# Kernel optimization log

Measured on AMD Instinct MI355X. Metric: run time of the kernel, lower is better.

## Reference

```python
import jax, jax.numpy as jnp
import numpy as np

IN_SIZE = 65536
HIDDEN = 128
D_STEPS = 64   # nd_actions[0]
N_ACT = 512    # nd_actions[1]


def setup_inputs() -> dict:
    key = jax.random.key(0)
    ks = jax.random.split(key, 7)
    s = 1.0 / np.sqrt(HIDDEN)  # torch LSTMCell/Linear init scale (uniform); use scaled normal
    return {
        "x": jax.random.normal(ks[0], (IN_SIZE,), jnp.float32),
        "w_ih": jax.random.normal(ks[1], (4 * HIDDEN, IN_SIZE), jnp.float32) * s,
        "w_hh": jax.random.normal(ks[2], (4 * HIDDEN, HIDDEN), jnp.float32) * s,
        "b_ih": jax.random.normal(ks[3], (4 * HIDDEN,), jnp.float32) * s,
        "b_hh": jax.random.normal(ks[4], (4 * HIDDEN,), jnp.float32) * s,
        "w_lin": jax.random.normal(ks[5], (N_ACT, HIDDEN), jnp.float32) * s,
        "b_lin": jax.random.normal(ks[6], (N_ACT,), jnp.float32) * s,
    }


def reference(x, w_ih, w_hh, b_ih, b_hh, w_lin, b_lin):
    # x is constant across the D steps, so its gate contribution is computed once.
    ihx = w_ih @ x + b_ih + b_hh  # (4H,)
    h0 = jnp.zeros((HIDDEN,), x.dtype)
    c0 = jnp.zeros((HIDDEN,), x.dtype)

    def step(carry, _):
        h, c = carry
        gates = ihx + w_hh @ h  # (4H,)
        i, f, g, o = jnp.split(gates, 4)  # torch LSTMCell gate order: i, f, g, o
        c = jax.nn.sigmoid(f) * c + jax.nn.sigmoid(i) * jnp.tanh(g)
        h = jax.nn.sigmoid(o) * jnp.tanh(c)
        logits = w_lin @ h + b_lin  # (N,)
        return (h, c), logits

    _, action_probs = jax.lax.scan(step, (h0, c0), None, length=D_STEPS)
    return action_probs  # (D, N)
```

## Files before the change

kernel.cpp:

```cpp
#include <hip/hip_runtime.h>
#include <hip/hip_bf16.h>

#define IN_SIZE 65536
#define HIDDEN 128
#define D_STEPS 64
#define N_ACT 512

typedef _Float16 half2_ __attribute__((ext_vector_type(2)));
typedef _Float16 half8_ __attribute__((ext_vector_type(8)));

__device__ __forceinline__ float dot2f(half2_ a, half2_ b, float c) {
#if __has_builtin(__builtin_amdgcn_fdot2)
    return __builtin_amdgcn_fdot2(a, b, c, false);
#else
    return c + (float)a[0] * (float)b[0] + (float)a[1] * (float)b[1];
#endif
}

__global__ __launch_bounds__(256) void k_ihx(const float* __restrict__ w_ih,
                                             const float* __restrict__ x,
                                             float* __restrict__ partials) {
    int bid = blockIdx.x;
    int rp = bid >> 3;
    int ck = bid & 7;
    int t = threadIdx.x;
    int r0 = 2 * rp, r1 = 2 * rp + 1;
    const float4* xp = (const float4*)(x + ck * 8192);
    const float4* w0 = (const float4*)(w_ih + (size_t)r0 * IN_SIZE + ck * 8192);
    const float4* w1 = (const float4*)(w_ih + (size_t)r1 * IN_SIZE + ck * 8192);

    float4 xv[8];
#pragma unroll
    for (int i = 0; i < 8; ++i) xv[i] = xp[t + i * 256];

    float a0 = 0.f, a1 = 0.f;
#pragma unroll
    for (int i = 0; i < 8; ++i) {
        float4 w4 = w0[t + i * 256];
        a0 += w4.x * xv[i].x + w4.y * xv[i].y + w4.z * xv[i].z + w4.w * xv[i].w;
    }
#pragma unroll
    for (int i = 0; i < 8; ++i) {
        float4 w4 = w1[t + i * 256];
        a1 += w4.x * xv[i].x + w4.y * xv[i].y + w4.z * xv[i].z + w4.w * xv[i].w;
    }
#pragma unroll
    for (int off = 32; off; off >>= 1) {
        a0 += __shfl_down(a0, off, 64);
        a1 += __shfl_down(a1, off, 64);
    }
    __shared__ float s[8];
    if ((t & 63) == 0) { s[t >> 6] = a0; s[4 + (t >> 6)] = a1; }
    __syncthreads();
    if (t == 0) {
        partials[r0 * 8 + ck] = s[0] + s[1] + s[2] + s[3];
        partials[r1 * 8 + ck] = s[4] + s[5] + s[6] + s[7];
    }
}

__global__ __launch_bounds__(512, 1) void k_rec_logits(
    const float* __restrict__ w_hh,
    const float* __restrict__ b_ih,
    const float* __restrict__ b_hh,
    const float* __restrict__ w_lin,
    const float* __restrict__ b_lin,
    const float* __restrict__ partials,
    float* __restrict__ out) {
    int t = threadIdx.x;
    int b = blockIdx.x;

    int gate = t & 3;
    int cell = t >> 2;
    int l = t & 63;
    int half = t & 1;

    __shared__ half8_ h_v[2][HIDDEN / 8];
    __shared__ float h_keep[HIDDEN];

    half2_ wrS[32], wrP[32];
    {
        int rowS_ = gate * HIDDEN + cell;
        int rowP_ = (gate ^ 1) * HIDDEN + cell;
        const float2* wpS = (const float2*)(w_hh + (size_t)rowS_ * HIDDEN + half * 64);
        const float2* wpP = (const float2*)(w_hh + (size_t)rowP_ * HIDDEN + half * 64);
#pragma unroll
        for (int i = 0; i < 32; ++i) {
            float2 vS = wpS[i], vP = wpP[i];
            half2_ a = {(_Float16)vS.x, (_Float16)vS.y};
            half2_ c2 = {(_Float16)vP.x, (_Float16)vP.y};
            wrS[i] = a; wrP[i] = c2;
        }
    }
    int rowS = gate * HIDDEN + cell;
    float ihx = b_ih[rowS] + b_hh[rowS];
#pragma unroll
    for (int pc = 0; pc < 8; ++pc) ihx += partials[rowS * 8 + pc];

    float c = 0.f;
    if (t < HIDDEN / 8) {
        half8_ z = {(_Float16)0.f, (_Float16)0.f, (_Float16)0.f, (_Float16)0.f,
                    (_Float16)0.f, (_Float16)0.f, (_Float16)0.f, (_Float16)0.f};
        h_v[0][t] = z;
    }
    __syncthreads();

    for (int d = 0; d < D_STEPS; ++d) {
        int rbuf = d & 1, wbuf = rbuf ^ 1;
        const half8_* hb = h_v[rbuf] + half * 8;
        float aS0 = 0.f, aS1 = 0.f, aP0 = 0.f, aP1 = 0.f;
#pragma unroll
        for (int i = 0; i < 8; ++i) {
            union { half8_ v8; half2_ p[4]; } u;
            u.v8 = hb[i];
            aS0 = dot2f(wrS[4 * i + 0], u.p[0], aS0);
            aS1 = dot2f(wrS[4 * i + 1], u.p[1], aS1);
            aS0 = dot2f(wrS[4 * i + 2], u.p[2], aS0);
            aS1 = dot2f(wrS[4 * i + 3], u.p[3], aS1);
            aP0 = dot2f(wrP[4 * i + 0], u.p[0], aP0);
            aP1 = dot2f(wrP[4 * i + 1], u.p[1], aP1);
            aP0 = dot2f(wrP[4 * i + 2], u.p[2], aP0);
            aP1 = dot2f(wrP[4 * i + 3], u.p[3], aP1);
        }
        float pS = aS0 + aS1;
        float pP = aP0 + aP1;
        float g = ihx + pS + __shfl_xor(pP, 1, 64);
        float kmul = (gate == 2) ? 2.f : 1.f;
        float sg = 1.f / (1.f + __expf(-kmul * g));
        float act = (gate == 2) ? (2.f * sg - 1.f) : sg;
        int base = l & ~3;
        float ai = __shfl(act, base + 0, 64);
        float af = __shfl(act, base + 1, 64);
        float at = __shfl(act, base + 2, 64);
        float ao = __shfl(act, base + 3, 64);
        c = af * c + ai * at;
        float h = ao * (2.f / (1.f + __expf(-2.f * c)) - 1.f);
        if ((t & 3) == 0) {
            ((_Float16*)&h_v[wbuf][0])[cell] = (_Float16)h;
            if (d == b) h_keep[cell] = h;
        }
        __syncthreads();
    }

    {
        const float4* wl = (const float4*)(w_lin + (size_t)t * HIDDEN);
        float acc = b_lin[t];
#pragma unroll
        for (int k = 0; k < HIDDEN / 4; ++k) {
            float4 w4 = wl[k];
            acc += w4.x * h_keep[4 * k + 0] + w4.y * h_keep[4 * k + 1] +
                   w4.z * h_keep[4 * k + 2] + w4.w * h_keep[4 * k + 3];
        }
        out[b * N_ACT + t] = acc;
    }
}

extern "C" void kernel_launch(void* const* d_in, const int* in_sizes, int n_in,
                              void* d_out, int out_size, void* d_ws, size_t ws_size,
                              hipStream_t stream) {
    const float* x     = (const float*)d_in[0];
    const float* w_ih  = (const float*)d_in[1];
    const float* w_hh  = (const float*)d_in[2];
    const float* b_ih  = (const float*)d_in[3];
    const float* b_hh  = (const float*)d_in[4];
    const float* w_lin = (const float*)d_in[5];
    const float* b_lin = (const float*)d_in[6];
    float* out = (float*)d_out;

    float* partials = (float*)d_ws;

    k_ihx<<<2048, 256, 0, stream>>>(w_ih, x, partials);
    k_rec_logits<<<D_STEPS, 512, 0, stream>>>(w_hh, b_ih, b_hh, w_lin, b_lin,
                                              partials, out);
}
```

Measured before the change: 79.43 us.

## Compute LSTM recurrent gate matvec with MFMA 16x16x32 f16 instructions

Replaces the per-thread fdot2 recurrent matvec with MFMA instructions. Each wave owns 16 hidden cells across all four gates and keeps the w_hh fragments as A operands in registers. The h vector is broadcast as the B operand, so each lane receives all four gates of its cells directly and the cross-lane shuffles for gate gathering disappear. The change also sets waves-per-EU attributes. It trades dot-product instruction count for MFMA latency on a tiny N=1 matvec, where most MFMA columns are wasted.

```diff
diff --git a/kernel.cpp b/kernel.cpp
--- a/kernel.cpp
+++ b/kernel.cpp
@@ -6,16 +6,9 @@
 #define D_STEPS 64
 #define N_ACT 512
 
-typedef _Float16 half2_ __attribute__((ext_vector_type(2)));
+typedef _Float16 half4_ __attribute__((ext_vector_type(4)));
 typedef _Float16 half8_ __attribute__((ext_vector_type(8)));
-
-__device__ __forceinline__ float dot2f(half2_ a, half2_ b, float c) {
-#if __has_builtin(__builtin_amdgcn_fdot2)
-    return __builtin_amdgcn_fdot2(a, b, c, false);
-#else
-    return c + (float)a[0] * (float)b[0] + (float)a[1] * (float)b[1];
-#endif
-}
+typedef float f32x4 __attribute__((ext_vector_type(4)));
 
 __global__ __launch_bounds__(256) void k_ihx(const float* __restrict__ w_ih,
                                              const float* __restrict__ x,
@@ -58,7 +51,9 @@
     }
 }
 
-__global__ __launch_bounds__(512, 1) void k_rec_logits(
+__global__ __attribute__((amdgpu_flat_work_group_size(512, 512)))
+__attribute__((amdgpu_waves_per_eu(2, 2)))
+void k_rec_logits(
     const float* __restrict__ w_hh,
     const float* __restrict__ b_ih,
     const float* __restrict__ b_hh,
@@ -68,75 +63,98 @@
     float* __restrict__ out) {
     int t = threadIdx.x;
     int b = blockIdx.x;
+    int w = t >> 6;
+    int l = t & 63;
+    int lg = l >> 4;
+    int lm = l & 15;
 
-    int gate = t & 3;
-    int cell = t >> 2;
-    int l = t & 63;
-    int half = t & 1;
-
-    __shared__ half8_ h_v[2][HIDDEN / 8];
+    __shared__ half8_ h_v[2][16];
     __shared__ float h_keep[HIDDEN];
 
-    half2_ wrS[32], wrP[32];
-    {
-        int rowS_ = gate * HIDDEN + cell;
-        int rowP_ = (gate ^ 1) * HIDDEN + cell;
-        const float2* wpS = (const float2*)(w_hh + (size_t)rowS_ * HIDDEN + half * 64);
-        const float2* wpP = (const float2*)(w_hh + (size_t)rowP_ * HIDDEN + half * 64);
+    half8_ afrag[4][4];
 #pragma unroll
-        for (int i = 0; i < 32; ++i) {
-            float2 vS = wpS[i], vP = wpP[i];
-            half2_ a = {(_Float16)vS.x, (_Float16)vS.y};
-            half2_ c2 = {(_Float16)vP.x, (_Float16)vP.y};
-            wrS[i] = a; wrP[i] = c2;
+    for (int G = 0; G < 4; ++G) {
+        const float* wrow = w_hh + (size_t)(G * HIDDEN + 16 * w + lm) * HIDDEN;
+#pragma unroll
+        for (int kt = 0; kt < 4; ++kt) {
+            const float4* wp = (const float4*)(wrow + kt * 32 + lg * 8);
+            float4 u0 = wp[0], u1 = wp[1];
+            half8_ a = {(_Float16)u0.x, (_Float16)u0.y, (_Float16)u0.z, (_Float16)u0.w,
+                        (_Float16)u1.x, (_Float16)u1.y, (_Float16)u1.z, (_Float16)u1.w};
+            afrag[G][kt] = a;
         }
     }
-    int rowS = gate * HIDDEN + cell;
-    float ihx = b_ih[rowS] + b_hh[rowS];
+    float ihx[4][4];
 #pragma unroll
-    for (int pc = 0; pc < 8; ++pc) ihx += partials[rowS * 8 + pc];
+    for (int G = 0; G < 4; ++G) {
+#pragma unroll
+        for (int r = 0; r < 4; ++r) {
+            int row = G * HIDDEN + 16 * w + lg * 4 + r;
+            const float4* pp = (const float4*)(partials + row * 8);
+            float4 p0 = pp[0], p1 = pp[1];
+            ihx[G][r] = p0.x + p0.y + p0.z + p0.w + p1.x + p1.y + p1.z + p1.w +
+                        b_ih[row] + b_hh[row];
+        }
+    }
 
-    float c = 0.f;
-    if (t < HIDDEN / 8) {
+    if (t < 16) {
         half8_ z = {(_Float16)0.f, (_Float16)0.f, (_Float16)0.f, (_Float16)0.f,
                     (_Float16)0.f, (_Float16)0.f, (_Float16)0.f, (_Float16)0.f};
         h_v[0][t] = z;
     }
     __syncthreads();
 
+    float c0 = 0.f, c1 = 0.f, c2 = 0.f, c3 = 0.f;
     for (int d = 0; d < D_STEPS; ++d) {
-        int rbuf = d & 1, wbuf = rbuf ^ 1;
-        const half8_* hb = h_v[rbuf] + half * 8;
-        float aS0 = 0.f, aS1 = 0.f, aP0 = 0.f, aP1 = 0.f;
+        int rb = d & 1, wb = rb ^ 1;
+        half8_ bf0 = h_v[rb][0 * 4 + lg];
+        half8_ bf1 = h_v[rb][1 * 4 + lg];
+        half8_ bf2 = h_v[rb][2 * 4 + lg];
+        half8_ bf3 = h_v[rb][3 * 4 + lg];
+
+        f32x4 ai_ = {ihx[0][0], ihx[0][1], ihx[0][2], ihx[0][3]};
+        f32x4 af_ = {ihx[1][0], ihx[1][1], ihx[1][2], ihx[1][3]};
+        f32x4 ag_ = {ihx[2][0], ihx[2][1], ihx[2][2], ihx[2][3]};
+        f32x4 ao_ = {ihx[3][0], ihx[3][1], ihx[3][2], ihx[3][3]};
+#define MFMA __builtin_amdgcn_mfma_f32_16x16x32_f16
+        ai_ = MFMA(afrag[0][0], bf0, ai_, 0, 0, 0);
+        af_ = MFMA(afrag[1][0], bf0, af_, 0, 0, 0);
+        ag_ = MFMA(afrag[2][0], bf0, ag_, 0, 0, 0);
+        ao_ = MFMA(afrag[3][0], bf0, ao_, 0, 0, 0);
+        ai_ = MFMA(afrag[0][1], bf1, ai_, 0, 0, 0);
+        af_ = MFMA(afrag[1][1], bf1, af_, 0, 0, 0);
+        ag_ = MFMA(afrag[2][1], bf1, ag_, 0, 0, 0);
+        ao_ = MFMA(afrag[3][1], bf1, ao_, 0, 0, 0);
+        ai_ = MFMA(afrag[0][2], bf2, ai_, 0, 0, 0);
+        af_ = MFMA(afrag[1][2], bf2, af_, 0, 0, 0);
+        ag_ = MFMA(afrag[2][2], bf2, ag_, 0, 0, 0);
+        ao_ = MFMA(afrag[3][2], bf2, ao_, 0, 0, 0);
+        ai_ = MFMA(afrag[0][3], bf3, ai_, 0, 0, 0);
+        af_ = MFMA(afrag[1][3], bf3, af_, 0, 0, 0);
+        ag_ = MFMA(afrag[2][3], bf3, ag_, 0, 0, 0);
+        ao_ = MFMA(afrag[3][3], bf3, ao_, 0, 0, 0);
+#undef MFMA
+        float hv[4];
 #pragma unroll
-        for (int i = 0; i < 8; ++i) {
-            union { half8_ v8; half2_ p[4]; } u;
-            u.v8 = hb[i];
-            aS0 = dot2f(wrS[4 * i + 0], u.p[0], aS0);
-            aS1 = dot2f(wrS[4 * i + 1], u.p[1], aS1);
-            aS0 = dot2f(wrS[4 * i + 2], u.p[2], aS0);
-            aS1 = dot2f(wrS[4 * i + 3], u.p[3], aS1);
-            aP0 = dot2f(wrP[4 * i + 0], u.p[0], aP0);
-            aP1 = dot2f(wrP[4 * i + 1], u.p[1], aP1);
-            aP0 = dot2f(wrP[4 * i + 2], u.p[2], aP0);
-            aP1 = dot2f(wrP[4 * i + 3], u.p[3], aP1);
+        for (int r = 0; r < 4; ++r) {
+            float ig = 1.f / (1.f + __expf(-ai_[r]));
+            float fg = 1.f / (1.f + __expf(-af_[r]));
+            float gg = 2.f / (1.f + __expf(-2.f * ag_[r])) - 1.f;
+            float og = 1.f / (1.f + __expf(-ao_[r]));
+            float* cp = (r == 0) ? &c0 : (r == 1) ? &c1 : (r == 2) ? &c2 : &c3;
+            float cn = fg * *cp + ig * gg;
+            *cp = cn;
+            hv[r] = og * (2.f / (1.f + __expf(-2.f * cn)) - 1.f);
         }
-        float pS = aS0 + aS1;
-        float pP = aP0 + aP1;
-        float g = ihx + pS + __shfl_xor(pP, 1, 64);
-        float kmul = (gate == 2) ? 2.f : 1.f;
-        float sg = 1.f / (1.f + __expf(-kmul * g));
-        float act = (gate == 2) ? (2.f * sg - 1.f) : sg;
-        int base = l & ~3;
-        float ai = __shfl(act, base + 0, 64);
-        float af = __shfl(act, base + 1, 64);
-        float at = __shfl(act, base + 2, 64);
-        float ao = __shfl(act, base + 3, 64);
-        c = af * c + ai * at;
-        float h = ao * (2.f / (1.f + __expf(-2.f * c)) - 1.f);
-        if ((t & 3) == 0) {
-            ((_Float16*)&h_v[wbuf][0])[cell] = (_Float16)h;
-            if (d == b) h_keep[cell] = h;
+        if (lm == 0) {
+            half4_ hp = {(_Float16)hv[0], (_Float16)hv[1],
+                         (_Float16)hv[2], (_Float16)hv[3]};
+            *(half4_*)((char*)(&h_v[wb][0]) + (size_t)(16 * w + lg * 4) * 2) = hp;
+            if (d == b) {
+                int cb = 16 * w + lg * 4;
+                h_keep[cb + 0] = hv[0]; h_keep[cb + 1] = hv[1];
+                h_keep[cb + 2] = hv[2]; h_keep[cb + 3] = hv[3];
+            }
         }
         __syncthreads();
     }
```

Result: slower. 135.1 us (+70.0%).
